# Performance work log

Hardware: AMD Instinct MI355X
Metric: run time of the kernel (lower is better)

## Reference

```python
import jax, jax.numpy as jnp
import numpy as np

EPS = 1e-3          # module eps
LAPLACE_EPS = 1e-5  # LaplaceModel eps
N_TAPS = 5
N_DELAY = 1
N_ITER = 5


def _mag_sq(x):
    return x.real ** 2 + x.imag ** 2


def _laplace_weights(Y):
    # LaplaceModel: r = 1 / clamp(2*sqrt(sum_f |Y|^2), eps), broadcast over freq
    denom = 2.0 * jnp.sqrt(jnp.sum(_mag_sq(Y), axis=-2, keepdims=True))
    w = 1.0 / jnp.maximum(denom, LAPLACE_EPS)
    return jnp.broadcast_to(w, Y.shape)


def _make_xbar(X):
    # X_bar[..., c, f, t, n] = X[..., c, f, n - (N_TAPS + N_DELAY) + t], zero-padded
    pad = N_TAPS + N_DELAY
    n_frames = X.shape[-1]
    pad_cfg = [(0, 0)] * (X.ndim - 1) + [(pad, 0)]
    Xp = jnp.pad(X, pad_cfg)
    taps = [Xp[..., t:t + n_frames] for t in range(N_TAPS)]
    return jnp.stack(taps, axis=-2)  # (..., n_chan, n_freq, n_taps, n_frames)


def _demix_derev(X, X_bar, W, H):
    reverb = jnp.einsum('...cfdt,...dftn->...cfn', H, X_bar)
    sep = jnp.einsum('...cfd,...dfn->...cfn', W, X)
    return sep - reverb


def _one_iter(Y, X_bar, W, H):
    n_src = Y.shape[-3]
    n_chan = X_bar.shape[-4]
    n_frames = Y.shape[-1]
    weights = _laplace_weights(Y)
    # rescaling step
    g = jnp.maximum(jnp.mean(_mag_sq(Y), axis=(-2, -1), keepdims=True), EPS)
    gs = jnp.sqrt(g)
    Y = Y / jnp.maximum(gs, EPS)
    W = W / jnp.maximum(gs, EPS)
    H = H / jnp.maximum(gs[..., None], EPS)
    weights = weights * g
    # ISS source updates (type 1)
    inv_nf = 1.0 / n_frames
    for src in range(n_src):
        Ys = Y[..., src, :, :]
        v_num = jnp.einsum('...cfn,...cfn,...fn->...cf', weights, Y, Ys.conj()) * inv_nf
        v_den = jnp.einsum('...cfn,...fn->...cf', weights, _mag_sq(Ys)) * inv_nf
        v = v_num / jnp.maximum(v_den, EPS)
        v_s = 1.0 - 1.0 / jnp.sqrt(jnp.maximum(v_den[..., src, :], EPS))
        v = v.at[..., src, :].set(v_s.astype(v.dtype))
        Y = Y - v[..., None] * Ys[..., None, :, :]
        W = W - jnp.einsum('...cf,...fd->...cfd', v, W[..., src, :, :])
        H = H - jnp.einsum('...cf,...fdt->...cfdt', v, H[..., src, :, :, :])
    # ISS tap updates (type 3)
    for src in range(n_chan):
        for tap in range(N_TAPS):
            Xst = X_bar[..., src, :, tap, :]
            v_num = jnp.einsum('...cfn,...cfn,...fn->...cf', weights, Y, Xst.conj())
            v_den = jnp.einsum('...cfn,...fn->...cf', weights, _mag_sq(Xst))
            v = v_num / jnp.maximum(v_den, EPS)
            Y = Y - v[..., None] * Xst[..., None, :, :]
            H = H.at[..., src, tap].add(v)
    return Y, W, H


def _forward(X):
    batch_shape = X.shape[:-3]
    n_chan, n_freq, n_frames = X.shape[-3:]
    n_src = n_chan  # determined case (n_src=None)
    X_bar = _make_xbar(X)
    eye = jnp.maximum(jnp.eye(n_src, n_chan, dtype=X.real.dtype), EPS)
    W = jnp.broadcast_to(eye[:, None, :].astype(X.dtype), batch_shape + (n_src, n_freq, n_chan))
    H = jnp.zeros(batch_shape + (n_src, n_freq, n_chan, N_TAPS), dtype=X.dtype)
    Y = _demix_derev(X, X_bar, W, H)
    for _ in range(N_ITER):
        Y, W, H = _one_iter(Y, X_bar, W, H)
    return jnp.stack([Y.real, Y.imag], axis=0)


def setup_inputs() -> dict:
    key = jax.random.key(0)
    k1, k2 = jax.random.split(key)
    shape = (2, 4, 512, 1000)  # (batch, n_chan, n_freq, n_frames)
    X_real = jax.random.normal(k1, shape, dtype=jnp.float32)
    X_imag = jax.random.normal(k2, shape, dtype=jnp.float32)
    return {"X_real": X_real, "X_imag": X_imag}


def reference(X_real, X_imag):
    X = jax.lax.complex(X_real, X_imag)
    return _forward(X)
```

## Files before the change

kernel.cpp:

```cpp
#include <hip/hip_runtime.h>


constexpr int NCH = 4;
constexpr int NFQ = 512;
constexpr int NFR = 1000;
constexpr int NIT = 5;
constexpr float EPSV  = 1e-3f;
constexpr float INVNF = 1.0f / 1000.0f;
constexpr float INVFN = 1.0f / (512.0f * 1000.0f);
constexpr size_t PLANE = 4096000;
constexpr size_t CSTRIDE = (size_t)NFQ * NFR;

typedef float f2 __attribute__((ext_vector_type(2)));

__device__ __forceinline__ float fast_rcp(float x) { return __builtin_amdgcn_rcpf(x); }
__device__ __forceinline__ float fast_rsq(float x) { return __builtin_amdgcn_rsqf(x); }

template <int CTRL>
__device__ __forceinline__ float dpp_add(float x) {
  return x + __int_as_float(__builtin_amdgcn_update_dpp(
      0, __float_as_int(x), CTRL, 0xF, 0xF, true));
}
__device__ __forceinline__ float wave_red(float x) {
  x = dpp_add<0xB1>(x);
  x = dpp_add<0x4E>(x);
  x = dpp_add<0x141>(x);
  x = dpp_add<0x140>(x);
  x = dpp_add<0x142>(x);
  x = dpp_add<0x143>(x);
  return __int_as_float(__builtin_amdgcn_readlane(__float_as_int(x), 63));
}

__device__ __forceinline__ f2 cmulconj(f2 y, f2 z) {
  f2 t, u;
  asm("v_pk_mul_f32 %0, %1, %2 op_sel:[1,1] op_sel_hi:[0,1] neg_hi:[1,0]"
      : "=v"(t) : "v"(y), "v"(z));
  asm("v_pk_fma_f32 %0, %1, %2, %3 op_sel_hi:[1,0,1]"
      : "=v"(u) : "v"(y), "v"(z), "v"(t));
  return u;
}
__device__ __forceinline__ void pk_acc(f2& p, f2 w2, f2 u) {
  asm("v_pk_fma_f32 %0, %1, %2, %0 op_sel_hi:[0,1,1]"
      : "+v"(p) : "v"(w2), "v"(u));
}
__device__ __forceinline__ void cupdate(f2& y, f2 v, f2 z) {
  asm("v_pk_fma_f32 %0, %1, %2, %0 op_sel_hi:[0,1,1] neg_lo:[1,0,0] neg_hi:[1,0,0]"
      : "+v"(y) : "v"(v), "v"(z));
  asm("v_pk_fma_f32 %0, %1, %2, %0 op_sel:[1,1,0] op_sel_hi:[1,0,1] neg_hi:[1,0,0]"
      : "+v"(y) : "v"(v), "v"(z));
}

__global__ __launch_bounds__(256, 4)
void init_y(const float* __restrict__ Xr, const float* __restrict__ Xi,
            float* __restrict__ Y, float* __restrict__ mag)
{
  const int bf = blockIdx.x, b = bf >> 9, f = bf & 511;
  const size_t base = ((size_t)b * NCH * NFQ + f) * NFR;
  const int tid = threadIdx.x;
  if (tid < 250) {
    const int nq = 4 * tid;
    float4 xr[4], xi[4];
    #pragma unroll
    for (int c = 0; c < 4; ++c) {
      xr[c] = *(const float4*)(Xr + base + (size_t)c * CSTRIDE + nq);
      xi[c] = *(const float4*)(Xi + base + (size_t)c * CSTRIDE + nq);
    }
    float4 sr, si;
    sr.x = xr[0].x+xr[1].x+xr[2].x+xr[3].x;  si.x = xi[0].x+xi[1].x+xi[2].x+xi[3].x;
    sr.y = xr[0].y+xr[1].y+xr[2].y+xr[3].y;  si.y = xi[0].y+xi[1].y+xi[2].y+xi[3].y;
    sr.z = xr[0].z+xr[1].z+xr[2].z+xr[3].z;  si.z = xi[0].z+xi[1].z+xi[2].z+xi[3].z;
    sr.w = xr[0].w+xr[1].w+xr[2].w+xr[3].w;  si.w = xi[0].w+xi[1].w+xi[2].w+xi[3].w;
    #pragma unroll
    for (int c = 0; c < 4; ++c) {
      float4 yr, yi;
      yr.x = 0.999f*xr[c].x + 0.001f*sr.x;  yi.x = 0.999f*xi[c].x + 0.001f*si.x;
      yr.y = 0.999f*xr[c].y + 0.001f*sr.y;  yi.y = 0.999f*xi[c].y + 0.001f*si.y;
      yr.z = 0.999f*xr[c].z + 0.001f*sr.z;  yi.z = 0.999f*xi[c].z + 0.001f*si.z;
      yr.w = 0.999f*xr[c].w + 0.001f*sr.w;  yi.w = 0.999f*xi[c].w + 0.001f*si.w;
      *(float4*)(Y + base + (size_t)c * CSTRIDE + nq)         = yr;
      *(float4*)(Y + base + (size_t)c * CSTRIDE + nq + PLANE) = yi;
      if (mag) {
        float4 m;
        m.x = yr.x*yr.x + yi.x*yi.x;  m.y = yr.y*yr.y + yi.y*yi.y;
        m.z = yr.z*yr.z + yi.z*yi.z;  m.w = yr.w*yr.w + yi.w*yi.w;
        *(float4*)(mag + base + (size_t)c * CSTRIDE + nq) = m;
      }
    }
  }
}

__global__ __launch_bounds__(256, 4)
void partial_mag(const float* __restrict__ mag, float* __restrict__ part2)
{
  const int id = blockIdx.x;
  const int k = id & 15, c = (id >> 4) & 3, b = id >> 6;
  const int tid = threadIdx.x;
  if (tid < 250) {
    const int nq = 4 * tid;
    const float* base = mag + ((size_t)((b*4+c)*NFQ + k*32)) * NFR + nq;
    float4 acc = make_float4(0.f, 0.f, 0.f, 0.f);
    for (int ff = 0; ff < 32; ++ff) {
      const float4 v = *(const float4*)(base + (size_t)ff * NFR);
      acc.x += v.x; acc.y += v.y; acc.z += v.z; acc.w += v.w;
    }
    *(float4*)(part2 + ((size_t)((b*4+c)*16 + k)) * NFR + nq) = acc;
  }
}

__global__ __launch_bounds__(256, 4)
void finish_mag(const float* __restrict__ part2, float* __restrict__ sumf)
{
  const int t = blockIdx.x * 256 + threadIdx.x;
  if (t < 2000) {
    const int b = t / 1000, r = t - 1000 * b;
    const int c = r / 250,  qn = r - 250 * c;
    const float* base = part2 + ((size_t)((b*4+c)*16)) * NFR + 4*qn;
    float4 acc = make_float4(0.f, 0.f, 0.f, 0.f);
    #pragma unroll
    for (int k = 0; k < 16; ++k) {
      const float4 v = *(const float4*)(base + (size_t)k * NFR);
      acc.x += v.x; acc.y += v.y; acc.z += v.z; acc.w += v.w;
    }
    *(float4*)(sumf + (size_t)b*4000 + c*1000 + 4*qn) = acc;
  }
}

__global__ __launch_bounds__(256, 4)
void partial_sumf(const float* __restrict__ Y, float* __restrict__ part)
{
  const int id = blockIdx.x;
  const int q = id & 31, c = (id >> 5) & 3, b = id >> 7;
  const size_t base = (size_t)(b * NCH + c) * CSTRIDE + (size_t)q * 16 * NFR;
  float acc[4] = {0.f, 0.f, 0.f, 0.f};
  for (int ff = 0; ff < 16; ++ff) {
    #pragma unroll
    for (int k = 0; k < 4; ++k) {
      const int n = threadIdx.x + 256 * k;
      if (n < NFR) {
        const float r = Y[base + (size_t)ff * NFR + n];
        const float i = Y[base + (size_t)ff * NFR + n + PLANE];
        acc[k] = fmaf(r, r, acc[k]);
        acc[k] = fmaf(i, i, acc[k]);
      }
    }
  }
  #pragma unroll
  for (int k = 0; k < 4; ++k) {
    const int n = threadIdx.x + 256 * k;
    if (n < NFR) part[((size_t)(b * NCH + c) * 32 + q) * NFR + n] = acc[k];
  }
}
__global__ __launch_bounds__(256, 4)
void finish_sumf(const float* __restrict__ part, float* __restrict__ sumf)
{
  const int o = blockIdx.x * 256 + threadIdx.x;
  if (o < 8000) {
    const int b = o / 4000;
    const int rem = o - b * 4000;
    const int c = rem / 1000;
    const int n = rem - c * 1000;
    const float* p = part + ((size_t)(b * NCH + c) * 32) * NFR + n;
    float s = 0.f;
    for (int q = 0; q < 32; ++q) s += p[(size_t)q * NFR];
    sumf[o] = s;
  }
}

__global__ __launch_bounds__(128, 2)
void iter_c(const float* __restrict__ Xr, const float* __restrict__ Xi,
            float* __restrict__ Y, const float* __restrict__ sumf,
            float* __restrict__ mag)
{
  __shared__ f2 x2[NCH][NFR];
  __shared__ float red[2][2][12];
  __shared__ float gred[2][4];

  const int tid  = threadIdx.x;
  const int lane = tid & 63;
  const int wid  = tid >> 6;
  const int ow   = wid ^ 1;
  const int bf   = blockIdx.x, b = bf >> 9, f = bf & 511;
  const size_t base = ((size_t)b * NCH * NFQ + f) * NFR;
  const int nb = 512 * wid + lane;

  for (int j = tid; j < NCH * 250; j += 128) {
    const int c = j / 250, q = j - c * 250;
    const float4 vr = *(const float4*)(Xr + base + (size_t)c*CSTRIDE + 4*q);
    const float4 vi = *(const float4*)(Xi + base + (size_t)c*CSTRIDE + 4*q);
    *(float4*)(&x2[c][4*q])     = make_float4(vr.x, vi.x, vr.y, vi.y);
    *(float4*)(&x2[c][4*q + 2]) = make_float4(vr.z, vi.z, vr.w, vi.w);
  }

  float w[8][4], invgs[4];
  {
    float sfr[8][4];
    const float* sfb = sumf + b * 4000;
    #pragma unroll
    for (int s = 0; s < 8; ++s) {
      const int na = min(nb + 64*s, 999);
      #pragma unroll
      for (int c = 0; c < 4; ++c) sfr[s][c] = sfb[c*1000 + na];
    }
    float gp[4] = {0.f, 0.f, 0.f, 0.f};
    #pragma unroll
    for (int s = 0; s < 8; ++s) {
      const bool valid = (nb + 64*s) < NFR;
      #pragma unroll
      for (int c = 0; c < 4; ++c) gp[c] += valid ? sfr[s][c] : 0.f;
    }
    #pragma unroll
    for (int c = 0; c < 4; ++c) gp[c] = wave_red(gp[c]);
    if (lane == 0) {
      #pragma unroll
      for (int c = 0; c < 4; ++c) gred[wid][c] = gp[c];
    }
    __syncthreads();

    #pragma unroll
    for (int c = 0; c < 4; ++c) {
      const float g = fmaxf((gred[0][c] + gred[1][c]) * INVFN, EPSV);
      invgs[c] = fast_rsq(g);
      #pragma unroll
      for (int s = 0; s < 8; ++s) {
        const bool valid = (nb + 64*s) < NFR;
        w[s][c] = valid ? g * fminf(0.5f * fast_rsq(sfr[s][c]), 1e5f) : 0.f;
      }
    }
  }

  f2 y2[8][4];
  #pragma unroll
  for (int s = 0; s < 8; ++s) {
    const int na = min(nb + 64*s, 999);
    #pragma unroll
    for (int c = 0; c < 4; ++c) {
      f2 t;
      t.x = Y[base + (size_t)c*CSTRIDE + na] * invgs[c];
      t.y = Y[base + (size_t)c*CSTRIDE + na + PLANE] * invgs[c];
      y2[s][c] = t;
    }
  }

  int par = 0;
  f2 p2[4]; float pd[4], vr_[4], vi_[4];

  #pragma unroll
  for (int src = 0; src < 4; ++src) {
    #pragma unroll
    for (int c = 0; c < 4; ++c) { p2[c] = (f2){0.f, 0.f}; pd[c] = 0.f; }
    #pragma unroll
    for (int s = 0; s < 8; ++s) {
      const f2 z = y2[s][src];
      const float zz = z.x*z.x + z.y*z.y;
      #pragma unroll
      for (int c = 0; c < 4; ++c) {
        const float wk = w[s][c];
        pd[c] = fmaf(wk, zz, pd[c]);
        if (c != src) {
          const f2 u = cmulconj(y2[s][c], z);
          f2 w2; w2.x = wk; w2.y = wk;
          pk_acc(p2[c], w2, u);
        }
      }
    }
    #pragma unroll
    for (int c = 0; c < 4; ++c) {
      pd[c] = wave_red(pd[c]);
      if (c != src) { p2[c].x = wave_red(p2[c].x); p2[c].y = wave_red(p2[c].y); }
    }
    if (lane == 0) {
      #pragma unroll
      for (int c = 0; c < 4; ++c) {
        red[par][wid][c]     = p2[c].x;
        red[par][wid][4 + c] = p2[c].y;
        red[par][wid][8 + c] = pd[c];
      }
    }
    __syncthreads();
    #pragma unroll
    for (int c = 0; c < 4; ++c) {
      p2[c].x += red[par][ow][c];
      p2[c].y += red[par][ow][4 + c];
      pd[c]   += red[par][ow][8 + c];
    }
    par ^= 1;

    f2 vp[4];
    #pragma unroll
    for (int c = 0; c < 4; ++c) {
      const float vd  = fmaxf(pd[c] * INVNF, EPSV);
      const float inv = INVNF * fast_rcp(vd);
      vr_[c] = p2[c].x * inv;  vi_[c] = p2[c].y * inv;
    }
    vr_[src] = 1.0f - fast_rsq(fmaxf(pd[src] * INVNF, EPSV));
    vi_[src] = 0.0f;
    #pragma unroll
    for (int c = 0; c < 4; ++c) { vp[c].x = vr_[c]; vp[c].y = vi_[c]; }

    #pragma unroll
    for (int s = 0; s < 8; ++s) {
      const f2 z = y2[s][src];
      #pragma unroll
      for (int c = 0; c < 4; ++c) cupdate(y2[s][c], vp[c], z);
    }
  }

  for (int src = 0; src < 4; ++src) {
    f2 xw[8][5];
    #pragma unroll
    for (int s = 0; s < 8; ++s) {
      #pragma unroll
      for (int o = 0; o < 5; ++o) {
        const int m = nb + 64*s - 6 + o;
        int mc = m;
        if (s == 0) mc = max(m, 0);
        if (s == 7) mc = min(m, 999);
        f2 v = x2[src][mc];
        if (s == 0 && m < 0) v = (f2){0.f, 0.f};
        xw[s][o] = v;
      }
    }

    #pragma unroll
    for (int tap = 0; tap < 5; ++tap) {
      #pragma unroll
      for (int c = 0; c < 4; ++c) { p2[c] = (f2){0.f, 0.f}; pd[c] = 0.f; }
      #pragma unroll
      for (int s = 0; s < 8; ++s) {
        const f2 z = xw[s][tap];
        const float zz = z.x*z.x + z.y*z.y;
        #pragma unroll
        for (int c = 0; c < 4; ++c) {
          const float wk = w[s][c];
          pd[c] = fmaf(wk, zz, pd[c]);
          const f2 u = cmulconj(y2[s][c], z);
          f2 w2; w2.x = wk; w2.y = wk;
          pk_acc(p2[c], w2, u);
        }
      }
      #pragma unroll
      for (int c = 0; c < 4; ++c) {
        p2[c].x = wave_red(p2[c].x);
        p2[c].y = wave_red(p2[c].y);
        pd[c]   = wave_red(pd[c]);
      }
      if (lane == 0) {
        #pragma unroll
        for (int c = 0; c < 4; ++c) {
          red[par][wid][c]     = p2[c].x;
          red[par][wid][4 + c] = p2[c].y;
          red[par][wid][8 + c] = pd[c];
        }
      }
      __syncthreads();
      #pragma unroll
      for (int c = 0; c < 4; ++c) {
        p2[c].x += red[par][ow][c];
        p2[c].y += red[par][ow][4 + c];
        pd[c]   += red[par][ow][8 + c];
      }
      par ^= 1;

      f2 vp[4];
      #pragma unroll
      for (int c = 0; c < 4; ++c) {
        const float inv = fast_rcp(fmaxf(pd[c], EPSV));
        vp[c].x = p2[c].x * inv;  vp[c].y = p2[c].y * inv;
      }
      #pragma unroll
      for (int s = 0; s < 8; ++s) {
        const f2 z = xw[s][tap];
        #pragma unroll
        for (int c = 0; c < 4; ++c) cupdate(y2[s][c], vp[c], z);
      }
    }
  }

  #pragma unroll
  for (int s = 0; s < 8; ++s) {
    const int n = nb + 64*s;
    if (n < NFR) {
      #pragma unroll
      for (int c = 0; c < 4; ++c) {
        const float yr = y2[s][c].x, yi = y2[s][c].y;
        Y[base + (size_t)c*CSTRIDE + n]         = yr;
        Y[base + (size_t)c*CSTRIDE + n + PLANE] = yi;
        if (mag) mag[base + (size_t)c*CSTRIDE + n] = yr*yr + yi*yi;
      }
    }
  }
}

extern "C" void kernel_launch(void* const* d_in, const int* in_sizes, int n_in,
                              void* d_out, int out_size, void* d_ws, size_t ws_size,
                              hipStream_t stream)
{
  const float* Xr = (const float*)d_in[0];
  const float* Xi = (const float*)d_in[1];
  float* Y = (float*)d_out;

  const bool big_ws = ws_size >= (size_t)(4096000 + 128000 + 8000) * 4;
  if (big_ws) {
    float* mag   = (float*)d_ws;
    float* part2 = mag + 4096000;
    float* sumf  = part2 + 128000;
    init_y<<<1024, 256, 0, stream>>>(Xr, Xi, Y, mag);
    for (int it = 0; it < NIT; ++it) {
      partial_mag<<<128, 256, 0, stream>>>(mag, part2);
      finish_mag<<<8, 256, 0, stream>>>(part2, sumf);
      iter_c<<<1024, 128, 0, stream>>>(Xr, Xi, Y, sumf,
                                       (it < NIT - 1) ? mag : nullptr);
    }
  } else {
    float* part = (float*)d_ws;
    float* sumf = part + 256000;
    init_y<<<1024, 256, 0, stream>>>(Xr, Xi, Y, nullptr);
    for (int it = 0; it < NIT; ++it) {
      partial_sumf<<<256, 256, 0, stream>>>(Y, part);
      finish_sumf<<<32, 256, 0, stream>>>(part, sumf);
      iter_c<<<1024, 128, 0, stream>>>(Xr, Xi, Y, sumf, nullptr);
    }
  }
}
```

Baseline: 305.1 us.

## Pair tap updates algebraically to halve block reductions and barriers in iter_c

Processes taps in pairs. Alongside the two tap correlations it accumulates the cross term between the two taps, so the second tap's update coefficient can be derived after the first update without a second reduction and barrier. This cuts the number of wave reductions and __syncthreads per source from five to three, in exchange for extra FMAs and more live registers (32 reduced values). It also moves the Y loads ahead of the X staging and weight computation so their latency overlaps that work.

```diff
diff --git a/kernel.cpp b/kernel.cpp
--- a/kernel.cpp
+++ b/kernel.cpp
@@ -172,7 +172,7 @@
             float* __restrict__ mag)
 {
   __shared__ f2 x2[NCH][NFR];
-  __shared__ float red[2][2][12];
+  __shared__ float red32[2][2][32];
   __shared__ float gred[2][4];
 
   const int tid  = threadIdx.x;
@@ -183,6 +183,19 @@
   const size_t base = ((size_t)b * NCH * NFQ + f) * NFR;
   const int nb = 512 * wid + lane;
 
+  f2 y2[8][4];
+  #pragma unroll
+  for (int s = 0; s < 8; ++s) {
+    const int na = min(nb + 64*s, 999);
+    #pragma unroll
+    for (int c = 0; c < 4; ++c) {
+      f2 t;
+      t.x = Y[base + (size_t)c*CSTRIDE + na];
+      t.y = Y[base + (size_t)c*CSTRIDE + na + PLANE];
+      y2[s][c] = t;
+    }
+  }
+
   for (int j = tid; j < NCH * 250; j += 128) {
     const int c = j / 250, q = j - c * 250;
     const float4 vr = *(const float4*)(Xr + base + (size_t)c*CSTRIDE + 4*q);
@@ -228,24 +241,20 @@
     }
   }
 
-  f2 y2[8][4];
   #pragma unroll
   for (int s = 0; s < 8; ++s) {
-    const int na = min(nb + 64*s, 999);
-    #pragma unroll
-    for (int c = 0; c < 4; ++c) {
-      f2 t;
-      t.x = Y[base + (size_t)c*CSTRIDE + na] * invgs[c];
-      t.y = Y[base + (size_t)c*CSTRIDE + na + PLANE] * invgs[c];
-      y2[s][c] = t;
+    #pragma unroll
+    for (int c = 0; c < 4; ++c) {
+      y2[s][c].x *= invgs[c];
+      y2[s][c].y *= invgs[c];
     }
   }
 
   int par = 0;
-  f2 p2[4]; float pd[4], vr_[4], vi_[4];
 
   #pragma unroll
   for (int src = 0; src < 4; ++src) {
+    f2 p2[4]; float pd[4];
     #pragma unroll
     for (int c = 0; c < 4; ++c) { p2[c] = (f2){0.f, 0.f}; pd[c] = 0.f; }
     #pragma unroll
@@ -271,17 +280,17 @@
     if (lane == 0) {
       #pragma unroll
       for (int c = 0; c < 4; ++c) {
-        red[par][wid][c]     = p2[c].x;
-        red[par][wid][4 + c] = p2[c].y;
-        red[par][wid][8 + c] = pd[c];
+        red32[par][wid][c]     = p2[c].x;
+        red32[par][wid][4 + c] = p2[c].y;
+        red32[par][wid][8 + c] = pd[c];
       }
     }
     __syncthreads();
     #pragma unroll
     for (int c = 0; c < 4; ++c) {
-      p2[c].x += red[par][ow][c];
-      p2[c].y += red[par][ow][4 + c];
-      pd[c]   += red[par][ow][8 + c];
+      p2[c].x += red32[par][ow][c];
+      p2[c].y += red32[par][ow][4 + c];
+      pd[c]   += red32[par][ow][8 + c];
     }
     par ^= 1;
 
@@ -290,12 +299,10 @@
     for (int c = 0; c < 4; ++c) {
       const float vd  = fmaxf(pd[c] * INVNF, EPSV);
       const float inv = INVNF * fast_rcp(vd);
-      vr_[c] = p2[c].x * inv;  vi_[c] = p2[c].y * inv;
-    }
-    vr_[src] = 1.0f - fast_rsq(fmaxf(pd[src] * INVNF, EPSV));
-    vi_[src] = 0.0f;
-    #pragma unroll
-    for (int c = 0; c < 4; ++c) { vp[c].x = vr_[c]; vp[c].y = vi_[c]; }
+      vp[c].x = p2[c].x * inv;  vp[c].y = p2[c].y * inv;
+    }
+    vp[src].x = 1.0f - fast_rsq(fmaxf(pd[src] * INVNF, EPSV));
+    vp[src].y = 0.0f;
 
     #pragma unroll
     for (int s = 0; s < 8; ++s) {
@@ -306,35 +313,115 @@
   }
 
   for (int src = 0; src < 4; ++src) {
-    f2 xw[8][5];
-    #pragma unroll
-    for (int s = 0; s < 8; ++s) {
-      #pragma unroll
-      for (int o = 0; o < 5; ++o) {
-        const int m = nb + 64*s - 6 + o;
+    #pragma unroll
+    for (int pr = 0; pr < 2; ++pr) {
+      f2 xwp[8][2];
+      #pragma unroll
+      for (int s = 0; s < 8; ++s) {
+        #pragma unroll
+        for (int j = 0; j < 2; ++j) {
+          const int m = nb + 64*s - 6 + 2*pr + j;
+          int mc = m;
+          if (s == 0) mc = max(m, 0);
+          if (s == 7) mc = min(m, 999);
+          f2 v = x2[src][mc];
+          if (s == 0 && m < 0) v = (f2){0.f, 0.f};
+          xwp[s][j] = v;
+        }
+      }
+
+      f2 p2a[4], p2b[4], px[4]; float pda[4], pdb[4];
+      #pragma unroll
+      for (int c = 0; c < 4; ++c) {
+        p2a[c] = (f2){0.f,0.f}; p2b[c] = (f2){0.f,0.f}; px[c] = (f2){0.f,0.f};
+        pda[c] = 0.f; pdb[c] = 0.f;
+      }
+      #pragma unroll
+      for (int s = 0; s < 8; ++s) {
+        const f2 za = xwp[s][0], zb = xwp[s][1];
+        const float zza = za.x*za.x + za.y*za.y;
+        const float zzb = zb.x*zb.x + zb.y*zb.y;
+        const f2 cab = cmulconj(za, zb);
+        #pragma unroll
+        for (int c = 0; c < 4; ++c) {
+          const float wk = w[s][c];
+          f2 w2; w2.x = wk; w2.y = wk;
+          pda[c] = fmaf(wk, zza, pda[c]);
+          pdb[c] = fmaf(wk, zzb, pdb[c]);
+          const f2 ua = cmulconj(y2[s][c], za);
+          pk_acc(p2a[c], w2, ua);
+          const f2 ub = cmulconj(y2[s][c], zb);
+          pk_acc(p2b[c], w2, ub);
+          pk_acc(px[c], w2, cab);
+        }
+      }
+
+      float rv[32];
+      #pragma unroll
+      for (int c = 0; c < 4; ++c) {
+        rv[c]      = p2a[c].x;  rv[4+c]  = p2a[c].y;  rv[8+c]  = pda[c];
+        rv[12+c]   = p2b[c].x;  rv[16+c] = p2b[c].y;  rv[20+c] = pdb[c];
+        rv[24+c]   = px[c].x;   rv[28+c] = px[c].y;
+      }
+      #pragma unroll
+      for (int j = 0; j < 32; ++j) rv[j] = wave_red(rv[j]);
+      if (lane == 0) {
+        #pragma unroll
+        for (int j = 0; j < 32; ++j) red32[par][wid][j] = rv[j];
+      }
+      __syncthreads();
+      #pragma unroll
+      for (int j = 0; j < 32; ++j) rv[j] += red32[par][ow][j];
+      par ^= 1;
+
+      f2 va[4], vb[4];
+      #pragma unroll
+      for (int c = 0; c < 4; ++c) {
+        const float inva = fast_rcp(fmaxf(rv[8+c], EPSV));
+        const float var = rv[c] * inva, vai = rv[4+c] * inva;
+        const float cxr = rv[24+c], cxi = rv[28+c];
+        const float nbr = rv[12+c] - (var*cxr - vai*cxi);
+        const float nbi = rv[16+c] - (var*cxi + vai*cxr);
+        const float invb = fast_rcp(fmaxf(rv[20+c], EPSV));
+        va[c].x = var;        va[c].y = vai;
+        vb[c].x = nbr * invb; vb[c].y = nbi * invb;
+      }
+      #pragma unroll
+      for (int s = 0; s < 8; ++s) {
+        const f2 za = xwp[s][0], zb = xwp[s][1];
+        #pragma unroll
+        for (int c = 0; c < 4; ++c) {
+          cupdate(y2[s][c], va[c], za);
+          cupdate(y2[s][c], vb[c], zb);
+        }
+      }
+    }
+
+    {
+      f2 xw4[8];
+      #pragma unroll
+      for (int s = 0; s < 8; ++s) {
+        const int m = nb + 64*s - 2;
         int mc = m;
         if (s == 0) mc = max(m, 0);
         if (s == 7) mc = min(m, 999);
         f2 v = x2[src][mc];
         if (s == 0 && m < 0) v = (f2){0.f, 0.f};
-        xw[s][o] = v;
-      }
-    }
-
-    #pragma unroll
-    for (int tap = 0; tap < 5; ++tap) {
-      #pragma unroll
-      for (int c = 0; c < 4; ++c) { p2[c] = (f2){0.f, 0.f}; pd[c] = 0.f; }
-      #pragma unroll
-      for (int s = 0; s < 8; ++s) {
-        const f2 z = xw[s][tap];
+        xw4[s] = v;
+      }
+      f2 p2[4]; float pd[4];
+      #pragma unroll
+      for (int c = 0; c < 4; ++c) { p2[c] = (f2){0.f,0.f}; pd[c] = 0.f; }
+      #pragma unroll
+      for (int s = 0; s < 8; ++s) {
+        const f2 z = xw4[s];
         const float zz = z.x*z.x + z.y*z.y;
         #pragma unroll
         for (int c = 0; c < 4; ++c) {
           const float wk = w[s][c];
+          f2 w2; w2.x = wk; w2.y = wk;
           pd[c] = fmaf(wk, zz, pd[c]);
           const f2 u = cmulconj(y2[s][c], z);
-          f2 w2; w2.x = wk; w2.y = wk;
           pk_acc(p2[c], w2, u);
         }
       }
@@ -347,17 +434,17 @@
       if (lane == 0) {
         #pragma unroll
         for (int c = 0; c < 4; ++c) {
-          red[par][wid][c]     = p2[c].x;
-          red[par][wid][4 + c] = p2[c].y;
-          red[par][wid][8 + c] = pd[c];
+          red32[par][wid][c]     = p2[c].x;
+          red32[par][wid][4 + c] = p2[c].y;
+          red32[par][wid][8 + c] = pd[c];
         }
       }
       __syncthreads();
       #pragma unroll
       for (int c = 0; c < 4; ++c) {
-        p2[c].x += red[par][ow][c];
-        p2[c].y += red[par][ow][4 + c];
-        pd[c]   += red[par][ow][8 + c];
+        p2[c].x += red32[par][ow][c];
+        p2[c].y += red32[par][ow][4 + c];
+        pd[c]   += red32[par][ow][8 + c];
       }
       par ^= 1;
 
@@ -369,7 +456,7 @@
       }
       #pragma unroll
       for (int s = 0; s < 8; ++s) {
-        const f2 z = xw[s][tap];
+        const f2 z = xw4[s];
         #pragma unroll
         for (int c = 0; c < 4; ++c) cupdate(y2[s][c], vp[c], z);
       }
```

New measurement: 330.5 us. 8.3% more time.
